# Kernel tuning notes

Measured on AMD Instinct MI355X. Metric: run time of the kernel, lower is better.

The kernel has to match this reference:

```python
import jax, jax.numpy as jnp
import numpy as np

B = 8192
I = 1024
H = 1024


def _xavier(key, out_dim, in_dim):
    limit = float(np.sqrt(6.0 / (in_dim + out_dim)))
    return jax.random.uniform(key, (out_dim, in_dim), jnp.float32, -limit, limit)


def setup_inputs() -> dict:
    key = jax.random.key(0)
    ks = jax.random.split(key, 16)
    inp = {
        "x": jax.random.normal(ks[0], (B, I), jnp.float32),
        "h_prev": jax.random.normal(ks[1], (B, H), jnp.float32),
        "c_prev": jax.random.normal(ks[2], (B, H), jnp.float32),
        # input->hidden weights (hidden_size, input_size), hidden->hidden (hidden_size, hidden_size)
        "Wxi": _xavier(ks[3], H, I), "Whi": _xavier(ks[4], H, H),
        "Wxf": _xavier(ks[5], H, I), "Whf": _xavier(ks[6], H, H),
        "Wxc": _xavier(ks[7], H, I), "Whc": _xavier(ks[8], H, H),
        "Wxo": _xavier(ks[9], H, I), "Who": _xavier(ks[10], H, H),
        "bxi": jnp.zeros((H,), jnp.float32), "bhi": jnp.zeros((H,), jnp.float32),
        # forget-gate biases initialized to ones per _init_weights
        "bxf": jnp.ones((H,), jnp.float32), "bhf": jnp.ones((H,), jnp.float32),
        "bxc": jnp.zeros((H,), jnp.float32), "bhc": jnp.zeros((H,), jnp.float32),
        "bxo": jnp.zeros((H,), jnp.float32), "bho": jnp.zeros((H,), jnp.float32),
    }
    return inp


def reference(x, h_prev, c_prev,
              Wxi, Whi, Wxf, Whf, Wxc, Whc, Wxo, Who,
              bxi, bhi, bxf, bhf, bxc, bhc, bxo, bho):
    # Fuse the 8 small linears into two GEMMs: stack along the output (gate) axis.
    Wx = jnp.concatenate([Wxi, Wxf, Wxc, Wxo], axis=0)   # (4H, I)
    Wh = jnp.concatenate([Whi, Whf, Whc, Who], axis=0)   # (4H, H)
    bx = jnp.concatenate([bxi, bxf, bxc, bxo], axis=0)    # (4H,)
    bh = jnp.concatenate([bhi, bhf, bhc, bho], axis=0)    # (4H,)
    gates = x @ Wx.T + h_prev @ Wh.T + (bx + bh)           # (B, 4H)
    zi, zf, zc, zo = jnp.split(gates, 4, axis=1)
    i = jax.nn.sigmoid(zi)
    f = jax.nn.sigmoid(zf)
    g = jnp.tanh(zc)
    o = jax.nn.sigmoid(zo)
    c_new = f * c_prev + i * g
    h_new = o * jnp.tanh(c_new)
    return (h_new, c_new)
```

## Files before the change

### kernel.cpp

```cpp
#include <hip/hip_runtime.h>
#include <hip/hip_bf16.h>
#include <stdint.h>


#define B_DIM 8192
#define I_DIM 1024
#define H_DIM 1024
#define K_DIM 2048
#define N_DIM 4096
#define NKT   32

typedef short bf16x8 __attribute__((ext_vector_type(8)));
typedef float f32x4 __attribute__((ext_vector_type(4)));

__device__ __forceinline__ unsigned short f2bf(float f) {
  unsigned int u = __float_as_uint(f);
  u += 0x7FFFu + ((u >> 16) & 1u);
  return (unsigned short)(u >> 16);
}

__global__ void pack_AB_kernel(const float* __restrict__ x, const float* __restrict__ h,
                               const float* __restrict__ Wxi, const float* __restrict__ Whi,
                               const float* __restrict__ Wxf, const float* __restrict__ Whf,
                               const float* __restrict__ Wxc, const float* __restrict__ Whc,
                               const float* __restrict__ Wxo, const float* __restrict__ Who,
                               unsigned short* __restrict__ outA,
                               unsigned short* __restrict__ outB) {
  const int totalA = B_DIM * K_DIM / 8;
  const int total  = totalA + N_DIM * K_DIM / 8;
  for (int idx = blockIdx.x * blockDim.x + threadIdx.x; idx < total;
       idx += gridDim.x * blockDim.x) {
    const float* src;
    unsigned short* dst;
    if (idx < totalA) {
      int row = idx >> 8;
      int col = (idx & 255) * 8;
      src = (col < I_DIM) ? (x + (size_t)row * I_DIM + col)
                          : (h + (size_t)row * H_DIM + (col - I_DIM));
      dst = outA + (size_t)idx * 8;
    } else {
      int u2 = idx - totalA;
      int r = u2 >> 8;
      int k = (u2 & 255) * 8;
      int g = (r >> 4) & 3;
      int hh = ((r >> 6) << 4) | (r & 15);
      src = (k < I_DIM)
          ? ((g == 0 ? Wxi : g == 1 ? Wxf : g == 2 ? Wxc : Wxo) + (size_t)hh * I_DIM + k)
          : ((g == 0 ? Whi : g == 1 ? Whf : g == 2 ? Whc : Who) + (size_t)hh * H_DIM + (k - I_DIM));
      dst = outB + (size_t)u2 * 8;
    }
    const float4* s4 = (const float4*)src;
    float4 v0 = s4[0], v1 = s4[1];
    bf16x8 o;
    o[0] = f2bf(v0.x); o[1] = f2bf(v0.y); o[2] = f2bf(v0.z); o[3] = f2bf(v0.w);
    o[4] = f2bf(v1.x); o[5] = f2bf(v1.y); o[6] = f2bf(v1.z); o[7] = f2bf(v1.w);
    *(bf16x8*)dst = o;
  }
}


#define STAGE(gptr, slotoff, ktile) do {                                          \
    int _ktc = (ktile) < NKT ? (ktile) : (NKT - 1);                               \
    const unsigned short* _g = (gptr) + (size_t)_ktc * 64;                        \
    __builtin_amdgcn_global_load_lds(                                             \
        (const __attribute__((address_space(1))) void*)_g,                        \
        (__attribute__((address_space(3))) void*)(lds + (slotoff) + wid * 1024),  \
        16, 0, 0);                                                                \
    __builtin_amdgcn_global_load_lds(                                             \
        (const __attribute__((address_space(1))) void*)(_g + (size_t)64 * K_DIM), \
        (__attribute__((address_space(3))) void*)(lds + (slotoff) + 8192 + wid * 1024), \
        16, 0, 0);                                                                \
  } while (0)

#define MFMAP(MH, AR, BR)                                                         \
  _Pragma("unroll") for (int mf = 0; mf < 4; ++mf)                                \
  _Pragma("unroll") for (int nn = 0; nn < 4; ++nn)                                \
    acc[(MH)*4 + mf][nn] = __builtin_amdgcn_mfma_f32_16x16x32_bf16(               \
        AR[mf], BR[nn], acc[(MH)*4 + mf][nn], 0, 0, 0)

#define RD_AQ(DST, MH, KOFF, BO)                                                  \
  _Pragma("unroll") for (int mf = 0; mf < 4; ++mf)                                \
    DST[mf] = *(const bf16x8*)(ldsAr + (BO) + (MH)*8192 + mf * 2048 + (KOFF));

#define RD_BH(DST, KOFF, BO)                                                      \
  _Pragma("unroll") for (int nn = 0; nn < 4; ++nn)                                \
    DST[nn] = *(const bf16x8*)(ldsBr + (BO) + nn * 2048 + (KOFF));

#define KTILE(BUF, KT) do {                                                       \
    const int _bo = (BUF) * 32768;                                                \
    const int _bo1 = ((BUF) ^ 1) * 32768;                                         \
                                          \
    __builtin_amdgcn_s_setprio(1);                                                \
    MFMAP(0, AQa, BHa);                                                           \
    __builtin_amdgcn_s_setprio(0);                                                \
    RD_AQ(AQb, 1, rd0, _bo);                                                      \
                                                                          \
    __builtin_amdgcn_s_setprio(1);                                                \
    MFMAP(1, AQb, BHa);                                                           \
    __builtin_amdgcn_s_setprio(0);                                                \
    RD_BH(BHb, rd1, _bo);                                                         \
    RD_AQ(AQa, 0, rd1, _bo);                                                      \
    __builtin_amdgcn_s_barrier();      \
        \
    __builtin_amdgcn_s_setprio(1);                                                \
    MFMAP(0, AQa, BHb);                                                           \
    __builtin_amdgcn_s_setprio(0);                                                \
    RD_AQ(AQb, 1, rd1, _bo);                                                      \
    STAGE(gB0p, 65536 + _bo, (KT) + 2);                                           \
    STAGE(gB1p, 65536 + _bo + 16384, (KT) + 2);                                   \
    asm volatile("s_waitcnt vmcnt(4)" ::: "memory");                              \
    __builtin_amdgcn_s_barrier();       \
               \
    __builtin_amdgcn_s_setprio(1);                                                \
    MFMAP(1, AQb, BHb);                                                           \
    __builtin_amdgcn_s_setprio(0);                                                \
    RD_AQ(AQa, 0, rd0, _bo1);                                                     \
    RD_BH(BHa, rd0, _bo1);                                                        \
    STAGE(gA0p, _bo, (KT) + 2);                                                   \
    STAGE(gA1p, _bo + 16384, (KT) + 2);                                           \
  } while (0)

__launch_bounds__(512, 2)
__global__ void lstm_gemm_kernel(const unsigned short* __restrict__ A,
                                 const unsigned short* __restrict__ Bp,
                                 const float* __restrict__ c_prev,
                                 const float* __restrict__ bxi, const float* __restrict__ bhi,
                                 const float* __restrict__ bxf, const float* __restrict__ bhf,
                                 const float* __restrict__ bxc, const float* __restrict__ bhc,
                                 const float* __restrict__ bxo, const float* __restrict__ bho,
                                 float* __restrict__ out) {
  __shared__ __align__(16) char lds[131072];

  const int nwg = gridDim.x;
  int bid = blockIdx.x;
  int q = nwg >> 3;
  int wg = (bid & 7) * q + (bid >> 3);
  int bm = wg >> 4;
  int bn = wg & 15;

  int tid = threadIdx.x;
  int lane = tid & 63;
  int wid = tid >> 6;
  int wm = wid >> 2;
  int wn = wid & 3;

  int srow = lane >> 3;
  int schunk = (lane & 7) ^ srow;
  const unsigned short* gA0p = A  + (size_t)(bm * 256 + wid * 8 + srow) * K_DIM + schunk * 8;
  const unsigned short* gA1p = gA0p + (size_t)128 * K_DIM;
  const unsigned short* gB0p = Bp + (size_t)(bn * 256 + wid * 8 + srow) * K_DIM + schunk * 8;
  const unsigned short* gB1p = gB0p + (size_t)128 * K_DIM;

  int c15 = lane & 15;
  int kl = lane >> 4;
  const char* ldsAr = lds + wm * 16384 + c15 * 128;
  const char* ldsBr = lds + 65536 + (wn >> 1) * 16384 + ((wn & 1) * 64 + c15) * 128;
  int rd0 = ((kl) ^ (lane & 7)) << 4;
  int rd1 = ((4 | kl) ^ (lane & 7)) << 4;

  f32x4 acc[8][4];
  f32x4 zero = {0.f, 0.f, 0.f, 0.f};
#pragma unroll
  for (int m = 0; m < 8; ++m)
#pragma unroll
    for (int n = 0; n < 4; ++n) acc[m][n] = zero;

  bf16x8 AQa[4], AQb[4];
  bf16x8 BHa[4], BHb[4];

  STAGE(gA0p, 0, 0);
  STAGE(gA1p, 16384, 0);
  STAGE(gB0p, 65536, 0);
  STAGE(gB1p, 65536 + 16384, 0);
  STAGE(gA0p, 32768, 1);
  STAGE(gA1p, 32768 + 16384, 1);
  STAGE(gB0p, 65536 + 32768, 1);
  STAGE(gB1p, 65536 + 32768 + 16384, 1);
  asm volatile("s_waitcnt vmcnt(8)" ::: "memory");
  __builtin_amdgcn_s_barrier();
  RD_AQ(AQa, 0, rd0, 0);
  RD_BH(BHa, rd0, 0);

#pragma unroll 1
  for (int kt = 0; kt < NKT; kt += 2) {
    KTILE(0, kt);
    KTILE(1, kt + 1);
  }

  int h = (bn * 4 + wn) * 16 + c15;
  float bi = bxi[h] + bhi[h];
  float bf_ = bxf[h] + bhf[h];
  float bc = bxc[h] + bhc[h];
  float bo = bxo[h] + bho[h];
  int row0 = bm * 256 + wm * 128 + kl * 4;
#pragma unroll
  for (int mi = 0; mi < 8; ++mi) {
#pragma unroll
    for (int j = 0; j < 4; ++j) {
      int r = row0 + mi * 16 + j;
      size_t off = (size_t)r * H_DIM + h;
      float zi = acc[mi][0][j] + bi;
      float zf = acc[mi][1][j] + bf_;
      float zc = acc[mi][2][j] + bc;
      float zo = acc[mi][3][j] + bo;
      float ig = 1.f / (1.f + __expf(-zi));
      float fg = 1.f / (1.f + __expf(-zf));
      float e2 = __expf(-2.f * zc);
      float gg = (1.f - e2) / (1.f + e2);
      float og = 1.f / (1.f + __expf(-zo));
      float cp = c_prev[off];
      float cn = fg * cp + ig * gg;
      float e2c = __expf(-2.f * cn);
      float th = (1.f - e2c) / (1.f + e2c);
      out[off] = og * th;
      out[(size_t)B_DIM * H_DIM + off] = cn;
    }
  }
}

extern "C" void kernel_launch(void* const* d_in, const int* in_sizes, int n_in,
                              void* d_out, int out_size, void* d_ws, size_t ws_size,
                              hipStream_t stream) {
  const float* x      = (const float*)d_in[0];
  const float* h_prev = (const float*)d_in[1];
  const float* c_prev = (const float*)d_in[2];
  const float* Wxi = (const float*)d_in[3];
  const float* Whi = (const float*)d_in[4];
  const float* Wxf = (const float*)d_in[5];
  const float* Whf = (const float*)d_in[6];
  const float* Wxc = (const float*)d_in[7];
  const float* Whc = (const float*)d_in[8];
  const float* Wxo = (const float*)d_in[9];
  const float* Who = (const float*)d_in[10];
  const float* bxi = (const float*)d_in[11];
  const float* bhi = (const float*)d_in[12];
  const float* bxf = (const float*)d_in[13];
  const float* bhf = (const float*)d_in[14];
  const float* bxc = (const float*)d_in[15];
  const float* bhc = (const float*)d_in[16];
  const float* bxo = (const float*)d_in[17];
  const float* bho = (const float*)d_in[18];

  unsigned short* Abf = (unsigned short*)d_ws;
  unsigned short* Bbf = (unsigned short*)((char*)d_ws + (size_t)B_DIM * K_DIM * 2);

  pack_AB_kernel<<<2048, 256, 0, stream>>>(x, h_prev,
      Wxi, Whi, Wxf, Whf, Wxc, Whc, Wxo, Who, Abf, Bbf);
  lstm_gemm_kernel<<<512, 512, 0, stream>>>(Abf, Bbf, c_prev,
      bxi, bhi, bxf, bhf, bxc, bhc, bxo, bho, (float*)d_out);
}
```

Measured before the change: 150.2 us.

## Switch GEMM to 32x32x16 MFMA tiles with lane-shuffled gate epilogue

```diff
diff --git a/kernel.cpp b/kernel.cpp
--- a/kernel.cpp
+++ b/kernel.cpp
@@ -11,7 +11,7 @@
 #define NKT   32
 
 typedef short bf16x8 __attribute__((ext_vector_type(8)));
-typedef float f32x4 __attribute__((ext_vector_type(4)));
+typedef float f32x16 __attribute__((ext_vector_type(16)));
 
 __device__ __forceinline__ unsigned short f2bf(float f) {
   unsigned int u = __float_as_uint(f);
@@ -72,50 +72,53 @@
         16, 0, 0);                                                                \
   } while (0)
 
-#define MFMAP(MH, AR, BR)                                                         \
-  _Pragma("unroll") for (int mf = 0; mf < 4; ++mf)                                \
-  _Pragma("unroll") for (int nn = 0; nn < 4; ++nn)                                \
-    acc[(MH)*4 + mf][nn] = __builtin_amdgcn_mfma_f32_16x16x32_bf16(               \
-        AR[mf], BR[nn], acc[(MH)*4 + mf][nn], 0, 0, 0)
-
-#define RD_AQ(DST, MH, KOFF, BO)                                                  \
-  _Pragma("unroll") for (int mf = 0; mf < 4; ++mf)                                \
-    DST[mf] = *(const bf16x8*)(ldsAr + (BO) + (MH)*8192 + mf * 2048 + (KOFF));
-
-#define RD_BH(DST, KOFF, BO)                                                      \
-  _Pragma("unroll") for (int nn = 0; nn < 4; ++nn)                                \
-    DST[nn] = *(const bf16x8*)(ldsBr + (BO) + nn * 2048 + (KOFF));
+#define MFMAP32(MH, AR, BR)                                                       \
+  _Pragma("unroll") for (int mf2 = 0; mf2 < 2; ++mf2)                             \
+  _Pragma("unroll") for (int nn = 0; nn < 2; ++nn)                                \
+  _Pragma("unroll") for (int kg2 = 0; kg2 < 2; ++kg2)                             \
+    acc[(MH)*2 + mf2][nn] = __builtin_amdgcn_mfma_f32_32x32x16_bf16(              \
+        AR[mf2*2 + kg2], BR[nn*2 + kg2], acc[(MH)*2 + mf2][nn], 0, 0, 0)
+
+#define RD_A32(DST, MH, KGP, BO)                                                  \
+  _Pragma("unroll") for (int mf2 = 0; mf2 < 2; ++mf2)                             \
+  _Pragma("unroll") for (int kg2 = 0; kg2 < 2; ++kg2)                             \
+    DST[mf2*2 + kg2] = *(const bf16x8*)(ldsAr + (BO) + ((MH)*2 + mf2) * 4096 + rdk[(KGP)*2 + kg2]);
+
+#define RD_B32(DST, KGP, BO)                                                      \
+  _Pragma("unroll") for (int nn = 0; nn < 2; ++nn)                                \
+  _Pragma("unroll") for (int kg2 = 0; kg2 < 2; ++kg2)                             \
+    DST[nn*2 + kg2] = *(const bf16x8*)(ldsBr + (BO) + nn * 4096 + rdk[(KGP)*2 + kg2]);
 
 #define KTILE(BUF, KT) do {                                                       \
     const int _bo = (BUF) * 32768;                                                \
     const int _bo1 = ((BUF) ^ 1) * 32768;                                         \
-                                          \
-    __builtin_amdgcn_s_setprio(1);                                                \
-    MFMAP(0, AQa, BHa);                                                           \
-    __builtin_amdgcn_s_setprio(0);                                                \
-    RD_AQ(AQb, 1, rd0, _bo);                                                      \
+                                                               \
+    __builtin_amdgcn_s_setprio(1);                                                \
+    MFMAP32(0, AQa, BHa);                                                         \
+    __builtin_amdgcn_s_setprio(0);                                                \
+    RD_A32(AQb, 1, 0, _bo);                                                       \
                                                                           \
     __builtin_amdgcn_s_setprio(1);                                                \
-    MFMAP(1, AQb, BHa);                                                           \
-    __builtin_amdgcn_s_setprio(0);                                                \
-    RD_BH(BHb, rd1, _bo);                                                         \
-    RD_AQ(AQa, 0, rd1, _bo);                                                      \
+    MFMAP32(1, AQb, BHa);                                                         \
+    __builtin_amdgcn_s_setprio(0);                                                \
+    RD_B32(BHb, 1, _bo);                                                          \
+    RD_A32(AQa, 0, 1, _bo);                                                       \
     __builtin_amdgcn_s_barrier();      \
         \
     __builtin_amdgcn_s_setprio(1);                                                \
-    MFMAP(0, AQa, BHb);                                                           \
-    __builtin_amdgcn_s_setprio(0);                                                \
-    RD_AQ(AQb, 1, rd1, _bo);                                                      \
+    MFMAP32(0, AQa, BHb);                                                         \
+    __builtin_amdgcn_s_setprio(0);                                                \
+    RD_A32(AQb, 1, 1, _bo);                                                       \
     STAGE(gB0p, 65536 + _bo, (KT) + 2);                                           \
     STAGE(gB1p, 65536 + _bo + 16384, (KT) + 2);                                   \
     asm volatile("s_waitcnt vmcnt(4)" ::: "memory");                              \
     __builtin_amdgcn_s_barrier();       \
-               \
-    __builtin_amdgcn_s_setprio(1);                                                \
-    MFMAP(1, AQb, BHb);                                                           \
-    __builtin_amdgcn_s_setprio(0);                                                \
-    RD_AQ(AQa, 0, rd0, _bo1);                                                     \
-    RD_BH(BHa, rd0, _bo1);                                                        \
+                                    \
+    __builtin_amdgcn_s_setprio(1);                                                \
+    MFMAP32(1, AQb, BHb);                                                         \
+    __builtin_amdgcn_s_setprio(0);                                                \
+    RD_A32(AQa, 0, 0, _bo1);                                                      \
+    RD_B32(BHa, 0, _bo1);                                                         \
     STAGE(gA0p, _bo, (KT) + 2);                                                   \
     STAGE(gA1p, _bo + 16384, (KT) + 2);                                           \
   } while (0)
@@ -151,19 +154,23 @@
   const unsigned short* gB0p = Bp + (size_t)(bn * 256 + wid * 8 + srow) * K_DIM + schunk * 8;
   const unsigned short* gB1p = gB0p + (size_t)128 * K_DIM;
 
-  int c15 = lane & 15;
-  int kl = lane >> 4;
-  const char* ldsAr = lds + wm * 16384 + c15 * 128;
-  const char* ldsBr = lds + 65536 + (wn >> 1) * 16384 + ((wn & 1) * 64 + c15) * 128;
-  int rd0 = ((kl) ^ (lane & 7)) << 4;
-  int rd1 = ((4 | kl) ^ (lane & 7)) << 4;
-
-  f32x4 acc[8][4];
-  f32x4 zero = {0.f, 0.f, 0.f, 0.f};
-#pragma unroll
-  for (int m = 0; m < 8; ++m)
-#pragma unroll
-    for (int n = 0; n < 4; ++n) acc[m][n] = zero;
+  int c31 = lane & 31;
+  int l7 = lane & 7;
+  int klane = lane >> 5;
+  const char* ldsAr = lds + wm * 16384 + c31 * 128;
+  const char* ldsBr = lds + 65536 + wn * 8192 + c31 * 128;
+  int rdk[4];
+#pragma unroll
+  for (int kg = 0; kg < 4; ++kg)
+    rdk[kg] = ((kg * 2 + klane) ^ l7) << 4;
+
+  f32x16 acc[4][2];
+#pragma unroll
+  for (int m = 0; m < 4; ++m)
+#pragma unroll
+    for (int n = 0; n < 2; ++n)
+#pragma unroll
+      for (int e = 0; e < 16; ++e) acc[m][n][e] = 0.f;
 
   bf16x8 AQa[4], AQb[4];
   bf16x8 BHa[4], BHb[4];
@@ -178,8 +185,8 @@
   STAGE(gB1p, 65536 + 32768 + 16384, 1);
   asm volatile("s_waitcnt vmcnt(8)" ::: "memory");
   __builtin_amdgcn_s_barrier();
-  RD_AQ(AQa, 0, rd0, 0);
-  RD_BH(BHa, rd0, 0);
+  RD_A32(AQa, 0, 0, 0);
+  RD_B32(BHa, 0, 0);
 
 #pragma unroll 1
   for (int kt = 0; kt < NKT; kt += 2) {
@@ -187,22 +194,28 @@
     KTILE(1, kt + 1);
   }
 
-  int h = (bn * 4 + wn) * 16 + c15;
+  int h = (bn * 4 + wn) * 16 + (lane & 15);
+  int bit16 = lane & 16;
   float bi = bxi[h] + bhi[h];
   float bf_ = bxf[h] + bhf[h];
   float bc = bxc[h] + bhc[h];
   float bo = bxo[h] + bho[h];
-  int row0 = bm * 256 + wm * 128 + kl * 4;
-#pragma unroll
-  for (int mi = 0; mi < 8; ++mi) {
-#pragma unroll
-    for (int j = 0; j < 4; ++j) {
-      int r = row0 + mi * 16 + j;
+  int row0 = bm * 256 + wm * 128 + 4 * (lane >> 5);
+  size_t outsel = bit16 ? (size_t)B_DIM * H_DIM : 0;
+#pragma unroll
+  for (int m = 0; m < 4; ++m) {
+#pragma unroll
+    for (int reg = 0; reg < 16; ++reg) {
+      int r = row0 + m * 32 + (reg & 3) + 8 * (reg >> 2);
       size_t off = (size_t)r * H_DIM + h;
-      float zi = acc[mi][0][j] + bi;
-      float zf = acc[mi][1][j] + bf_;
-      float zc = acc[mi][2][j] + bc;
-      float zo = acc[mi][3][j] + bo;
+      float o0 = acc[m][0][reg];
+      float o1 = acc[m][1][reg];
+      float x0 = __shfl_xor(o0, 16);
+      float x1 = __shfl_xor(o1, 16);
+      float zi = (bit16 ? x0 : o0) + bi;
+      float zf = (bit16 ? o0 : x0) + bf_;
+      float zc = (bit16 ? x1 : o1) + bc;
+      float zo = (bit16 ? o1 : x1) + bo;
       float ig = 1.f / (1.f + __expf(-zi));
       float fg = 1.f / (1.f + __expf(-zf));
       float e2 = __expf(-2.f * zc);
@@ -212,8 +225,8 @@
       float cn = fg * cp + ig * gg;
       float e2c = __expf(-2.f * cn);
       float th = (1.f - e2c) / (1.f + e2c);
-      out[off] = og * th;
-      out[(size_t)B_DIM * H_DIM + off] = cn;
+      float hv = og * th;
+      out[off + outsel] = bit16 ? cn : hv;
     }
   }
 }
```

Result: slower. 188.3 us (+25.4%).
